# Performance work log

Measured on AMD Instinct MI355X. Metric: run time of the kernel, lower is better.

Reference implementation:

```python
import jax, jax.numpy as jnp
import numpy as np

N_HEADS = 16
HEAD_DIM = 128


def _rotate_half(x):
    x1, x2 = jnp.split(x, 2, axis=-1)
    return jnp.concatenate((-x2, x1), axis=-1)


def setup_inputs() -> dict:
    key = jax.random.key(0)
    ks = jax.random.split(key, 6)
    B, T, D = 2, 2048, 2048
    d = D // N_HEADS  # 128
    x = jax.random.normal(ks[0], (B, T, D), dtype=jnp.float32)
    # RoPE tables (shape [1,1,T,head_dim]) built as in standard implementations
    inv_freq = 1.0 / (10000.0 ** (jnp.arange(0, d, 2, dtype=jnp.float32) / d))
    ang = jnp.arange(T, dtype=jnp.float32)[:, None] * inv_freq[None, :]  # [T, d/2]
    emb = jnp.concatenate((ang, ang), axis=-1)  # [T, d]
    rope_cos = jnp.cos(emb)[None, None]
    rope_sin = jnp.sin(emb)[None, None]
    qkv_w = jax.random.normal(ks[1], (3 * D, D), dtype=jnp.float32) * (1.0 / np.sqrt(D))
    qkv_b = jnp.zeros((3 * D,), dtype=jnp.float32)
    out_w = jax.random.normal(ks[2], (D, D), dtype=jnp.float32) * (1.0 / np.sqrt(D))
    out_b = jnp.zeros((D,), dtype=jnp.float32)
    return {"x": x, "rope_cos": rope_cos, "rope_sin": rope_sin,
            "qkv_w": qkv_w, "qkv_b": qkv_b, "out_w": out_w, "out_b": out_b}


def reference(x, rope_cos, rope_sin, qkv_w, qkv_b, out_w, out_b):
    B, T, D = x.shape
    H, d = N_HEADS, D // N_HEADS
    # fused QKV projection: [B,T,3D] -> [3,B,H,T,d]
    qkv = (jnp.einsum('btd,ed->bte', x, qkv_w) + qkv_b)
    qkv = qkv.reshape(B, T, 3, H, d).transpose(2, 0, 3, 1, 4)
    q, k, v = qkv[0], qkv[1], qkv[2]
    cos = rope_cos[:, :, :T, :].astype(q.dtype)
    sin = rope_sin[:, :, :T, :].astype(q.dtype)
    q = q * cos + _rotate_half(q) * sin
    k = k * cos + _rotate_half(k) * sin
    # causal SDPA
    scale = 1.0 / jnp.sqrt(jnp.array(d, dtype=q.dtype))
    scores = jnp.einsum('bhqd,bhkd->bhqk', q, k) * scale  # [B,H,T,T]
    causal = jnp.tril(jnp.ones((T, T), dtype=bool))
    scores = jnp.where(causal, scores, jnp.finfo(scores.dtype).min)
    attn = jax.nn.softmax(scores, axis=-1)
    out = jnp.einsum('bhqk,bhkd->bhqd', attn, v)  # [B,H,T,d]
    out = out.transpose(0, 2, 1, 3).reshape(B, T, D)
    return jnp.einsum('btd,ed->bte', out, out_w) + out_b
```

## Files before the change

kernel.cpp:

```cpp
#include <hip/hip_runtime.h>
#include <cstdint>
#include <cstddef>

typedef unsigned short u16;
using bf16x8 = __attribute__((ext_vector_type(8))) short;
using f32x4  = __attribute__((ext_vector_type(4))) float;

#define MFMA16(a, b, c) __builtin_amdgcn_mfma_f32_16x16x32_bf16((a), (b), (c), 0, 0, 0)

__device__ __forceinline__ u16 f2bf(float f) {
  union { float f; unsigned u; } x; x.f = f;
  unsigned r = x.u + 0x7fffu + ((x.u >> 16) & 1u);
  return (u16)(r >> 16);
}
__device__ __forceinline__ float bf2f(u16 h) {
  union { unsigned u; float f; } x; x.u = ((unsigned)h) << 16;
  return x.f;
}
__device__ __forceinline__ void gll16(const void* g, void* l) {
  __builtin_amdgcn_global_load_lds((const __attribute__((address_space(1))) void*)g,
                                   (__attribute__((address_space(3))) void*)l, 16, 0, 0);
}

union U8 { bf16x8 v; u16 u[8]; };

__global__ __launch_bounds__(256) void cvt_kernel(const float* __restrict__ in,
                                                  u16* __restrict__ out, int n4) {
  int i = blockIdx.x * blockDim.x + threadIdx.x;
  if (i >= n4) return;
  float4 v = ((const float4*)in)[i];
  ushort4 o;
  o.x = f2bf(v.x); o.y = f2bf(v.y); o.z = f2bf(v.z); o.w = f2bf(v.w);
  ((ushort4*)out)[i] = o;
}

__global__ __launch_bounds__(256) void gemm_bt(const u16* __restrict__ A,
                                               const u16* __restrict__ Bw,
                                               const float* __restrict__ bias,
                                               void* __restrict__ Cout,
                                               int M, int N, int K, int out_bf16) {
  __shared__ u16 As[128 * 32];
  __shared__ u16 Bs[128 * 32];
  const int tid = threadIdx.x;
  const int lane = tid & 63, wave = tid >> 6;
  const int col = lane & 15, quad = lane >> 4;
  const int wr = wave >> 1, wc = wave & 1;
  const int bm = blockIdx.y, bn = blockIdx.x;
  const u16* Ag = A + (size_t)bm * 128 * K;
  const u16* Bg = Bw + (size_t)bn * 128 * K;
  f32x4 acc[4][4] = {};
  const int r0 = tid >> 2, kc = (tid & 3) * 8;
  for (int k0 = 0; k0 < K; k0 += 32) {
    __syncthreads();
    gll16(Ag + (size_t)r0 * K + k0 + kc,        (void*)(As + (size_t)tid * 8));
    gll16(Ag + (size_t)(r0 + 64) * K + k0 + kc, (void*)(As + (size_t)(256 + tid) * 8));
    gll16(Bg + (size_t)r0 * K + k0 + kc,        (void*)(Bs + (size_t)tid * 8));
    gll16(Bg + (size_t)(r0 + 64) * K + k0 + kc, (void*)(Bs + (size_t)(256 + tid) * 8));
    __syncthreads();
    bf16x8 af[4], bf[4];
#pragma unroll
    for (int i = 0; i < 4; i++) {
      af[i] = *(const bf16x8*)&As[(wr * 64 + i * 16 + col) * 32 + quad * 8];
      bf[i] = *(const bf16x8*)&Bs[(wc * 64 + i * 16 + col) * 32 + quad * 8];
    }
#pragma unroll
    for (int i = 0; i < 4; i++)
#pragma unroll
      for (int j = 0; j < 4; j++)
        acc[i][j] = MFMA16(af[i], bf[j], acc[i][j]);
  }
#pragma unroll
  for (int i = 0; i < 4; i++) {
    int row0 = bm * 128 + wr * 64 + i * 16 + quad * 4;
#pragma unroll
    for (int j = 0; j < 4; j++) {
      int cn = bn * 128 + wc * 64 + j * 16 + col;
      float bv = bias[cn];
#pragma unroll
      for (int r = 0; r < 4; r++) {
        float v = acc[i][j][r] + bv;
        size_t off = (size_t)(row0 + r) * N + cn;
        if (out_bf16) ((u16*)Cout)[off] = f2bf(v);
        else          ((float*)Cout)[off] = v;
      }
    }
  }
}

__global__ __launch_bounds__(256) void rope_kernel(const u16* __restrict__ qkv,
                                                   const float* __restrict__ cosT,
                                                   const float* __restrict__ sinT,
                                                   u16* __restrict__ qo,
                                                   u16* __restrict__ ko,
                                                   u16* __restrict__ vt) {
  __shared__ u16 vs[128 * 72];
  const int bh = blockIdx.x;
  const int b = bh >> 4, h = bh & 15;
  const int tb = blockIdx.y;
  const int tid = threadIdx.x;
  const int tl = tid >> 2;
  const int g = tid & 3;
  const int t = tb * 64 + tl;
  const size_t qrow = ((size_t)(b * 2048 + t)) * 6144 + h * 128;
  const size_t orow = ((size_t)bh * 2048 + t) * 128;
  const int tt = t * 128;
  const int dl = g * 16, dh = 64 + dl;
  const float scale = 0.08838834764831845f;
#pragma unroll
  for (int cch = 0; cch < 2; cch++) {
    const int o8 = cch * 8;
    U8 ql, qh, kl, kh, vl, vh;
    ql.v = *(const bf16x8*)&qkv[qrow + dl + o8];
    qh.v = *(const bf16x8*)&qkv[qrow + dh + o8];
    kl.v = *(const bf16x8*)&qkv[qrow + 2048 + dl + o8];
    kh.v = *(const bf16x8*)&qkv[qrow + 2048 + dh + o8];
    vl.v = *(const bf16x8*)&qkv[qrow + 4096 + dl + o8];
    vh.v = *(const bf16x8*)&qkv[qrow + 4096 + dh + o8];
    float cl[8], ch_[8], sl[8], sh_[8];
    *(float4*)&cl[0]  = *(const float4*)&cosT[tt + dl + o8];
    *(float4*)&cl[4]  = *(const float4*)&cosT[tt + dl + o8 + 4];
    *(float4*)&ch_[0] = *(const float4*)&cosT[tt + dh + o8];
    *(float4*)&ch_[4] = *(const float4*)&cosT[tt + dh + o8 + 4];
    *(float4*)&sl[0]  = *(const float4*)&sinT[tt + dl + o8];
    *(float4*)&sl[4]  = *(const float4*)&sinT[tt + dl + o8 + 4];
    *(float4*)&sh_[0] = *(const float4*)&sinT[tt + dh + o8];
    *(float4*)&sh_[4] = *(const float4*)&sinT[tt + dh + o8 + 4];
    U8 aq, bq, ak, bk;
#pragma unroll
    for (int i = 0; i < 8; i++) {
      float qlf = bf2f(ql.u[i]), qhf = bf2f(qh.u[i]);
      float klf = bf2f(kl.u[i]), khf = bf2f(kh.u[i]);
      aq.u[i] = f2bf((qlf * cl[i]  - qhf * sl[i])  * scale);
      bq.u[i] = f2bf((qhf * ch_[i] + qlf * sh_[i]) * scale);
      ak.u[i] = f2bf(klf * cl[i]  - khf * sl[i]);
      bk.u[i] = f2bf(khf * ch_[i] + klf * sh_[i]);
    }
    *(bf16x8*)&qo[orow + dl + o8] = aq.v;
    *(bf16x8*)&qo[orow + dh + o8] = bq.v;
    *(bf16x8*)&ko[orow + dl + o8] = ak.v;
    *(bf16x8*)&ko[orow + dh + o8] = bk.v;
#pragma unroll
    for (int i = 0; i < 8; i++) {
      vs[(dl + o8 + i) * 72 + tl] = vl.u[i];
      vs[(dh + o8 + i) * 72 + tl] = vh.u[i];
    }
  }
  __syncthreads();
#pragma unroll
  for (int c = 0; c < 4; c++) {
    int idx = c * 256 + tid;
    int dd = idx >> 3, chk = idx & 7;
    bf16x8 vv = *(const bf16x8*)&vs[dd * 72 + chk * 8];
    *(bf16x8*)&vt[((size_t)bh * 128 + dd) * 2048 + tb * 64 + chk * 8] = vv;
  }
}

__global__ __launch_bounds__(256) void attn_kernel(const u16* __restrict__ Q,
                                                   const u16* __restrict__ Kk,
                                                   const u16* __restrict__ Vt,
                                                   u16* __restrict__ O) {
  __shared__ u16 Ks[64 * 136];
  __shared__ u16 Vs[128 * 72];
  __shared__ u16 Ps[4][16 * 72];
  const int bh = blockIdx.y, b = bh >> 4, h = bh & 15;
  const int qtile = gridDim.x - 1 - blockIdx.x;
  const int qb = qtile * 128;
  const int tid = threadIdx.x, wave = tid >> 6, lane = tid & 63;
  const int col = lane & 15, quad = lane >> 4;
  const int qw0 = qb + wave * 32;
  const int qw1 = qw0 + 16;
  const u16* Qg = Q + (size_t)bh * 2048 * 128;
  const u16* Kg = Kk + (size_t)bh * 2048 * 128;
  const u16* Vg = Vt + (size_t)bh * 128 * 2048;
  bf16x8 qf0[4], qf1[4];
#pragma unroll
  for (int c = 0; c < 4; c++) {
    qf0[c] = *(const bf16x8*)&Qg[(size_t)(qw0 + col) * 128 + c * 32 + quad * 8];
    qf1[c] = *(const bf16x8*)&Qg[(size_t)(qw1 + col) * 128 + c * 32 + quad * 8];
  }
  f32x4 o0[8] = {}, o1[8] = {};
  float ls0[4] = {0.f, 0.f, 0.f, 0.f}, ls1[4] = {0.f, 0.f, 0.f, 0.f};
  const int ntiles = (qb + 128) >> 6;
  const int kr = tid >> 2, kc = (tid & 3) * 8;
  const int vr = tid >> 1, vc = (tid & 1) * 8;
  for (int it = 0; it < ntiles; ++it) {
    const int kt = it << 6;
    __syncthreads();
#pragma unroll
    for (int u = 0; u < 4; u++)
      *(bf16x8*)&Ks[kr * 136 + kc + u * 32] =
          *(const bf16x8*)&Kg[(size_t)(kt + kr) * 128 + kc + u * 32];
#pragma unroll
    for (int u = 0; u < 4; u++)
      *(bf16x8*)&Vs[vr * 72 + vc + u * 16] =
          *(const bf16x8*)&Vg[(size_t)vr * 2048 + kt + vc + u * 16];
    __syncthreads();
    if (kt > qw1 + 15) continue;
    const bool do0 = (kt <= qw0 + 15);
    f32x4 s0[4] = {}, s1[4] = {};
#pragma unroll
    for (int c = 0; c < 4; c++) {
#pragma unroll
      for (int kg = 0; kg < 4; kg++) {
        bf16x8 kf = *(const bf16x8*)&Ks[(kg * 16 + col) * 136 + c * 32 + quad * 8];
        s0[kg] = MFMA16(qf0[c], kf, s0[kg]);
        s1[kg] = MFMA16(qf1[c], kf, s1[kg]);
      }
    }
    u16* pw = Ps[wave];
    if (do0) {
#pragma unroll
      for (int kg = 0; kg < 4; kg++)
#pragma unroll
        for (int r = 0; r < 4; r++) {
          int key = kt + kg * 16 + col, qg = qw0 + quad * 4 + r;
          float p = (key <= qg) ? __expf(s0[kg][r]) : 0.f;
          ls0[r] += p;
          pw[(quad * 4 + r) * 72 + kg * 16 + col] = f2bf(p);
        }
#pragma unroll
      for (int ks = 0; ks < 64; ks += 32) {
        bf16x8 pf = *(const bf16x8*)&pw[col * 72 + ks + quad * 8];
#pragma unroll
        for (int dt = 0; dt < 8; dt++) {
          bf16x8 vf = *(const bf16x8*)&Vs[(dt * 16 + col) * 72 + ks + quad * 8];
          o0[dt] = MFMA16(pf, vf, o0[dt]);
        }
      }
    }
    {
#pragma unroll
      for (int kg = 0; kg < 4; kg++)
#pragma unroll
        for (int r = 0; r < 4; r++) {
          int key = kt + kg * 16 + col, qg = qw1 + quad * 4 + r;
          float p = (key <= qg) ? __expf(s1[kg][r]) : 0.f;
          ls1[r] += p;
          pw[(quad * 4 + r) * 72 + kg * 16 + col] = f2bf(p);
        }
#pragma unroll
      for (int ks = 0; ks < 64; ks += 32) {
        bf16x8 pf = *(const bf16x8*)&pw[col * 72 + ks + quad * 8];
#pragma unroll
        for (int dt = 0; dt < 8; dt++) {
          bf16x8 vf = *(const bf16x8*)&Vs[(dt * 16 + col) * 72 + ks + quad * 8];
          o1[dt] = MFMA16(pf, vf, o1[dt]);
        }
      }
    }
  }
#pragma unroll
  for (int st = 1; st < 16; st <<= 1)
#pragma unroll
    for (int r = 0; r < 4; r++) {
      ls0[r] += __shfl_xor(ls0[r], st);
      ls1[r] += __shfl_xor(ls1[r], st);
    }
#pragma unroll
  for (int r = 0; r < 4; r++) {
    float inv0 = 1.0f / ls0[r], inv1 = 1.0f / ls1[r];
    size_t row0 = ((size_t)(b * 2048 + qw0 + quad * 4 + r)) * 2048 + h * 128;
    size_t row1 = ((size_t)(b * 2048 + qw1 + quad * 4 + r)) * 2048 + h * 128;
#pragma unroll
    for (int dt = 0; dt < 8; dt++) {
      O[row0 + dt * 16 + col] = f2bf(o0[dt][r] * inv0);
      O[row1 + dt * 16 + col] = f2bf(o1[dt][r] * inv1);
    }
  }
}

extern "C" void kernel_launch(void* const* d_in, const int* in_sizes, int n_in,
                              void* d_out, int out_size, void* d_ws, size_t ws_size,
                              hipStream_t stream) {
  const float* x        = (const float*)d_in[0];
  const float* rope_cos = (const float*)d_in[1];
  const float* rope_sin = (const float*)d_in[2];
  const float* qkv_w    = (const float*)d_in[3];
  const float* qkv_b    = (const float*)d_in[4];
  const float* out_w    = (const float*)d_in[5];
  const float* out_b    = (const float*)d_in[6];
  float* out = (float*)d_out;
  u16* ws = (u16*)d_ws;
  u16* xb    = ws;
  u16* wqkvb = xb + 8388608;
  u16* woutb = wqkvb + 12582912;
  u16* qkvb  = woutb + 4194304;
  u16* qb    = qkvb + 25165824;
  u16* kb    = qb + 8388608;
  u16* vtb   = kb + 8388608;
  u16* attnb = xb;

  cvt_kernel<<<8192, 256, 0, stream>>>(x, xb, 2097152);
  cvt_kernel<<<12288, 256, 0, stream>>>(qkv_w, wqkvb, 3145728);
  cvt_kernel<<<4096, 256, 0, stream>>>(out_w, woutb, 1048576);
  gemm_bt<<<dim3(48, 32), 256, 0, stream>>>(xb, wqkvb, qkv_b, qkvb, 4096, 6144, 2048, 1);
  rope_kernel<<<dim3(32, 32), 256, 0, stream>>>(qkvb, rope_cos, rope_sin, qb, kb, vtb);
  attn_kernel<<<dim3(16, 32), 256, 0, stream>>>(qb, kb, vtb, attnb);
  gemm_bt<<<dim3(16, 32), 256, 0, stream>>>(attnb, woutb, out_b, out, 4096, 2048, 2048, 0);
}
```

Measured before the change: 466.4 us.

## Fuse RoPE and V transpose into QKV GEMM epilogue, merge casts, interleave PV MFMAs

The separate rope kernel is removed. The QKV GEMM epilogue now stages each 128x128 tile in shared memory, applies RoPE and the softmax scale for Q and K, and writes V transposed directly. This avoids writing and re-reading the bf16 QKV intermediate. The three fp32-to-bf16 casts are merged into one launch. In attention, both P fragments are built first so each V fragment load feeds two MFMAs, which halves the V LDS reads. The cost is a heavier GEMM epilogue and higher register pressure in the attention loop.

```diff
diff --git a/kernel.cpp b/kernel.cpp
--- a/kernel.cpp
+++ b/kernel.cpp
@@ -24,21 +24,139 @@
 
 union U8 { bf16x8 v; u16 u[8]; };
 
-__global__ __launch_bounds__(256) void cvt_kernel(const float* __restrict__ in,
-                                                  u16* __restrict__ out, int n4) {
+__global__ __launch_bounds__(256) void cvt3_kernel(const float* __restrict__ a, u16* __restrict__ oa, int na4,
+                                                   const float* __restrict__ bsrc, u16* __restrict__ ob, int nb4,
+                                                   const float* __restrict__ c, u16* __restrict__ oc, int nc4) {
   int i = blockIdx.x * blockDim.x + threadIdx.x;
-  if (i >= n4) return;
-  float4 v = ((const float4*)in)[i];
+  const float4* in; ushort4* out;
+  if (i < na4) { in = (const float4*)a + i; out = (ushort4*)oa + i; }
+  else if (i < na4 + nb4) { int j = i - na4; in = (const float4*)bsrc + j; out = (ushort4*)ob + j; }
+  else if (i < na4 + nb4 + nc4) { int j = i - na4 - nb4; in = (const float4*)c + j; out = (ushort4*)oc + j; }
+  else return;
+  float4 v = *in;
   ushort4 o;
   o.x = f2bf(v.x); o.y = f2bf(v.y); o.z = f2bf(v.z); o.w = f2bf(v.w);
-  ((ushort4*)out)[i] = o;
+  *out = o;
+}
+
+__global__ __launch_bounds__(256) void gemm_qkv_rope(const u16* __restrict__ A,
+                                                     const u16* __restrict__ Bw,
+                                                     const float* __restrict__ bias,
+                                                     const float* __restrict__ cosT,
+                                                     const float* __restrict__ sinT,
+                                                     u16* __restrict__ qo,
+                                                     u16* __restrict__ ko,
+                                                     u16* __restrict__ vt) {
+  __shared__ u16 smem[128 * 136];
+  u16* As = smem;
+  u16* Bs = smem + 8192;
+  const int K = 2048;
+  const int tid = threadIdx.x;
+  const int lane = tid & 63, wave = tid >> 6;
+  const int col = lane & 15, quad = lane >> 4;
+  const int wr = wave >> 1, wc = wave & 1;
+  const int bm = blockIdx.y, bn = blockIdx.x;
+  const u16* Ag = A + (size_t)bm * 128 * K;
+  const u16* Bg = Bw + (size_t)bn * 128 * K;
+  f32x4 acc[4][4] = {};
+  const int r0 = tid >> 2, kc = (tid & 3) * 8;
+  for (int k0 = 0; k0 < K; k0 += 32) {
+    __syncthreads();
+    gll16(Ag + (size_t)r0 * K + k0 + kc,        (void*)(As + (size_t)tid * 8));
+    gll16(Ag + (size_t)(r0 + 64) * K + k0 + kc, (void*)(As + (size_t)(256 + tid) * 8));
+    gll16(Bg + (size_t)r0 * K + k0 + kc,        (void*)(Bs + (size_t)tid * 8));
+    gll16(Bg + (size_t)(r0 + 64) * K + k0 + kc, (void*)(Bs + (size_t)(256 + tid) * 8));
+    __syncthreads();
+    bf16x8 af[4], bf[4];
+#pragma unroll
+    for (int i = 0; i < 4; i++) {
+      af[i] = *(const bf16x8*)&As[(wr * 64 + i * 16 + col) * 32 + quad * 8];
+      bf[i] = *(const bf16x8*)&Bs[(wc * 64 + i * 16 + col) * 32 + quad * 8];
+    }
+#pragma unroll
+    for (int i = 0; i < 4; i++)
+#pragma unroll
+      for (int j = 0; j < 4; j++)
+        acc[i][j] = MFMA16(af[i], bf[j], acc[i][j]);
+  }
+  const int proj = bn >> 4, h = bn & 15;
+  const int bloc = bm >> 4;
+  const int tbase = (bm & 15) * 128;
+  const size_t bh = (size_t)(bloc * 16 + h);
+  __syncthreads();
+  if (proj < 2) {
+#pragma unroll
+    for (int i = 0; i < 4; i++) {
+      int tr = wr * 64 + i * 16 + quad * 4;
+#pragma unroll
+      for (int j = 0; j < 4; j++) {
+        int cf = wc * 64 + j * 16 + col;
+        float bv = bias[bn * 128 + cf];
+#pragma unroll
+        for (int r = 0; r < 4; r++)
+          smem[(tr + r) * 136 + cf] = f2bf(acc[i][j][r] + bv);
+      }
+    }
+    __syncthreads();
+    const int t_l = tid >> 1, hseg = (tid & 1) * 32;
+    const int t = tbase + t_l;
+    u16* dst = proj ? ko : qo;
+    const float scale = proj ? 1.0f : 0.08838834764831845f;
+    size_t orow = (bh * 2048 + t) * 128;
+#pragma unroll
+    for (int c4 = 0; c4 < 4; c4++) {
+      int d0 = hseg + c4 * 8;
+      U8 lo, hi, olo, ohi;
+      lo.v = *(const bf16x8*)&smem[t_l * 136 + d0];
+      hi.v = *(const bf16x8*)&smem[t_l * 136 + d0 + 64];
+      float cl[8], ch_[8], sl[8], sh_[8];
+      *(float4*)&cl[0]  = *(const float4*)&cosT[t * 128 + d0];
+      *(float4*)&cl[4]  = *(const float4*)&cosT[t * 128 + d0 + 4];
+      *(float4*)&ch_[0] = *(const float4*)&cosT[t * 128 + d0 + 64];
+      *(float4*)&ch_[4] = *(const float4*)&cosT[t * 128 + d0 + 68];
+      *(float4*)&sl[0]  = *(const float4*)&sinT[t * 128 + d0];
+      *(float4*)&sl[4]  = *(const float4*)&sinT[t * 128 + d0 + 4];
+      *(float4*)&sh_[0] = *(const float4*)&sinT[t * 128 + d0 + 64];
+      *(float4*)&sh_[4] = *(const float4*)&sinT[t * 128 + d0 + 68];
+#pragma unroll
+      for (int e = 0; e < 8; e++) {
+        float l = bf2f(lo.u[e]), hv = bf2f(hi.u[e]);
+        olo.u[e] = f2bf((l * cl[e] - hv * sl[e]) * scale);
+        ohi.u[e] = f2bf((hv * ch_[e] + l * sh_[e]) * scale);
+      }
+      *(bf16x8*)&dst[orow + d0] = olo.v;
+      *(bf16x8*)&dst[orow + d0 + 64] = ohi.v;
+    }
+  } else {
+#pragma unroll
+    for (int i = 0; i < 4; i++) {
+      int t0 = wr * 64 + i * 16 + quad * 4;
+#pragma unroll
+      for (int j = 0; j < 4; j++) {
+        int d = wc * 64 + j * 16 + col;
+        float bv = bias[bn * 128 + d];
+        ushort4 pk;
+        pk.x = f2bf(acc[i][j][0] + bv);
+        pk.y = f2bf(acc[i][j][1] + bv);
+        pk.z = f2bf(acc[i][j][2] + bv);
+        pk.w = f2bf(acc[i][j][3] + bv);
+        *(ushort4*)&smem[d * 136 + t0] = pk;
+      }
+    }
+    __syncthreads();
+    const int d_l = tid >> 1, tseg = (tid & 1) * 64;
+    size_t vrow = (bh * 128 + d_l) * 2048 + tbase + tseg;
+#pragma unroll
+    for (int c8 = 0; c8 < 8; c8++)
+      *(bf16x8*)&vt[vrow + c8 * 8] = *(const bf16x8*)&smem[d_l * 136 + tseg + c8 * 8];
+  }
 }
 
 __global__ __launch_bounds__(256) void gemm_bt(const u16* __restrict__ A,
                                                const u16* __restrict__ Bw,
                                                const float* __restrict__ bias,
-                                               void* __restrict__ Cout,
-                                               int M, int N, int K, int out_bf16) {
+                                               float* __restrict__ Cout,
+                                               int M, int N, int K) {
   __shared__ u16 As[128 * 32];
   __shared__ u16 Bs[128 * 32];
   const int tid = threadIdx.x;
@@ -77,81 +195,9 @@
       int cn = bn * 128 + wc * 64 + j * 16 + col;
       float bv = bias[cn];
 #pragma unroll
-      for (int r = 0; r < 4; r++) {
-        float v = acc[i][j][r] + bv;
-        size_t off = (size_t)(row0 + r) * N + cn;
-        if (out_bf16) ((u16*)Cout)[off] = f2bf(v);
-        else          ((float*)Cout)[off] = v;
-      }
-    }
-  }
-}
-
-__global__ __launch_bounds__(256) void rope_kernel(const u16* __restrict__ qkv,
-                                                   const float* __restrict__ cosT,
-                                                   const float* __restrict__ sinT,
-                                                   u16* __restrict__ qo,
-                                                   u16* __restrict__ ko,
-                                                   u16* __restrict__ vt) {
-  __shared__ u16 vs[128 * 72];
-  const int bh = blockIdx.x;
-  const int b = bh >> 4, h = bh & 15;
-  const int tb = blockIdx.y;
-  const int tid = threadIdx.x;
-  const int tl = tid >> 2;
-  const int g = tid & 3;
-  const int t = tb * 64 + tl;
-  const size_t qrow = ((size_t)(b * 2048 + t)) * 6144 + h * 128;
-  const size_t orow = ((size_t)bh * 2048 + t) * 128;
-  const int tt = t * 128;
-  const int dl = g * 16, dh = 64 + dl;
-  const float scale = 0.08838834764831845f;
-#pragma unroll
-  for (int cch = 0; cch < 2; cch++) {
-    const int o8 = cch * 8;
-    U8 ql, qh, kl, kh, vl, vh;
-    ql.v = *(const bf16x8*)&qkv[qrow + dl + o8];
-    qh.v = *(const bf16x8*)&qkv[qrow + dh + o8];
-    kl.v = *(const bf16x8*)&qkv[qrow + 2048 + dl + o8];
-    kh.v = *(const bf16x8*)&qkv[qrow + 2048 + dh + o8];
-    vl.v = *(const bf16x8*)&qkv[qrow + 4096 + dl + o8];
-    vh.v = *(const bf16x8*)&qkv[qrow + 4096 + dh + o8];
-    float cl[8], ch_[8], sl[8], sh_[8];
-    *(float4*)&cl[0]  = *(const float4*)&cosT[tt + dl + o8];
-    *(float4*)&cl[4]  = *(const float4*)&cosT[tt + dl + o8 + 4];
-    *(float4*)&ch_[0] = *(const float4*)&cosT[tt + dh + o8];
-    *(float4*)&ch_[4] = *(const float4*)&cosT[tt + dh + o8 + 4];
-    *(float4*)&sl[0]  = *(const float4*)&sinT[tt + dl + o8];
-    *(float4*)&sl[4]  = *(const float4*)&sinT[tt + dl + o8 + 4];
-    *(float4*)&sh_[0] = *(const float4*)&sinT[tt + dh + o8];
-    *(float4*)&sh_[4] = *(const float4*)&sinT[tt + dh + o8 + 4];
-    U8 aq, bq, ak, bk;
-#pragma unroll
-    for (int i = 0; i < 8; i++) {
-      float qlf = bf2f(ql.u[i]), qhf = bf2f(qh.u[i]);
-      float klf = bf2f(kl.u[i]), khf = bf2f(kh.u[i]);
-      aq.u[i] = f2bf((qlf * cl[i]  - qhf * sl[i])  * scale);
-      bq.u[i] = f2bf((qhf * ch_[i] + qlf * sh_[i]) * scale);
-      ak.u[i] = f2bf(klf * cl[i]  - khf * sl[i]);
-      bk.u[i] = f2bf(khf * ch_[i] + klf * sh_[i]);
-    }
-    *(bf16x8*)&qo[orow + dl + o8] = aq.v;
-    *(bf16x8*)&qo[orow + dh + o8] = bq.v;
-    *(bf16x8*)&ko[orow + dl + o8] = ak.v;
-    *(bf16x8*)&ko[orow + dh + o8] = bk.v;
-#pragma unroll
-    for (int i = 0; i < 8; i++) {
-      vs[(dl + o8 + i) * 72 + tl] = vl.u[i];
-      vs[(dh + o8 + i) * 72 + tl] = vh.u[i];
-    }
-  }
-  __syncthreads();
-#pragma unroll
-  for (int c = 0; c < 4; c++) {
-    int idx = c * 256 + tid;
-    int dd = idx >> 3, chk = idx & 7;
-    bf16x8 vv = *(const bf16x8*)&vs[dd * 72 + chk * 8];
-    *(bf16x8*)&vt[((size_t)bh * 128 + dd) * 2048 + tb * 64 + chk * 8] = vv;
+      for (int r = 0; r < 4; r++)
+        Cout[(size_t)(row0 + r) * N + cn] = acc[i][j][r] + bv;
+    }
   }
 }
 
@@ -208,6 +254,7 @@
       }
     }
     u16* pw = Ps[wave];
+    bf16x8 pf0[2], pf1[2];
     if (do0) {
 #pragma unroll
       for (int kg = 0; kg < 4; kg++)
@@ -218,35 +265,37 @@
           ls0[r] += p;
           pw[(quad * 4 + r) * 72 + kg * 16 + col] = f2bf(p);
         }
-#pragma unroll
-      for (int ks = 0; ks < 64; ks += 32) {
-        bf16x8 pf = *(const bf16x8*)&pw[col * 72 + ks + quad * 8];
+      pf0[0] = *(const bf16x8*)&pw[col * 72 + quad * 8];
+      pf0[1] = *(const bf16x8*)&pw[col * 72 + 32 + quad * 8];
+    }
+#pragma unroll
+    for (int kg = 0; kg < 4; kg++)
+#pragma unroll
+      for (int r = 0; r < 4; r++) {
+        int key = kt + kg * 16 + col, qg = qw1 + quad * 4 + r;
+        float p = (key <= qg) ? __expf(s1[kg][r]) : 0.f;
+        ls1[r] += p;
+        pw[(quad * 4 + r) * 72 + kg * 16 + col] = f2bf(p);
+      }
+    pf1[0] = *(const bf16x8*)&pw[col * 72 + quad * 8];
+    pf1[1] = *(const bf16x8*)&pw[col * 72 + 32 + quad * 8];
+    if (do0) {
+#pragma unroll
+      for (int ks = 0; ks < 2; ks++)
 #pragma unroll
         for (int dt = 0; dt < 8; dt++) {
-          bf16x8 vf = *(const bf16x8*)&Vs[(dt * 16 + col) * 72 + ks + quad * 8];
-          o0[dt] = MFMA16(pf, vf, o0[dt]);
+          bf16x8 vf = *(const bf16x8*)&Vs[(dt * 16 + col) * 72 + ks * 32 + quad * 8];
+          o0[dt] = MFMA16(pf0[ks], vf, o0[dt]);
+          o1[dt] = MFMA16(pf1[ks], vf, o1[dt]);
         }
-      }
-    }
-    {
-#pragma unroll
-      for (int kg = 0; kg < 4; kg++)
-#pragma unroll
-        for (int r = 0; r < 4; r++) {
-          int key = kt + kg * 16 + col, qg = qw1 + quad * 4 + r;
-          float p = (key <= qg) ? __expf(s1[kg][r]) : 0.f;
-          ls1[r] += p;
-          pw[(quad * 4 + r) * 72 + kg * 16 + col] = f2bf(p);
+    } else {
+#pragma unroll
+      for (int ks = 0; ks < 2; ks++)
+#pragma unroll
+        for (int dt = 0; dt < 8; dt++) {
+          bf16x8 vf = *(const bf16x8*)&Vs[(dt * 16 + col) * 72 + ks * 32 + quad * 8];
+          o1[dt] = MFMA16(pf1[ks], vf, o1[dt]);
         }
-#pragma unroll
-      for (int ks = 0; ks < 64; ks += 32) {
-        bf16x8 pf = *(const bf16x8*)&pw[col * 72 + ks + quad * 8];
-#pragma unroll
-        for (int dt = 0; dt < 8; dt++) {
-          bf16x8 vf = *(const bf16x8*)&Vs[(dt * 16 + col) * 72 + ks + quad * 8];
-          o1[dt] = MFMA16(pf, vf, o1[dt]);
-        }
-      }
     }
   }
 #pragma unroll
@@ -284,17 +333,16 @@
   u16* xb    = ws;
   u16* wqkvb = xb + 8388608;
   u16* woutb = wqkvb + 12582912;
-  u16* qkvb  = woutb + 4194304;
-  u16* qb    = qkvb + 25165824;
+  u16* qb    = woutb + 4194304;
   u16* kb    = qb + 8388608;
   u16* vtb   = kb + 8388608;
   u16* attnb = xb;
 
-  cvt_kernel<<<8192, 256, 0, stream>>>(x, xb, 2097152);
-  cvt_kernel<<<12288, 256, 0, stream>>>(qkv_w, wqkvb, 3145728);
-  cvt_kernel<<<4096, 256, 0, stream>>>(out_w, woutb, 1048576);
-  gemm_bt<<<dim3(48, 32), 256, 0, stream>>>(xb, wqkvb, qkv_b, qkvb, 4096, 6144, 2048, 1);
-  rope_kernel<<<dim3(32, 32), 256, 0, stream>>>(qkvb, rope_cos, rope_sin, qb, kb, vtb);
+  cvt3_kernel<<<24576, 256, 0, stream>>>(x, xb, 2097152,
+                                         qkv_w, wqkvb, 3145728,
+                                         out_w, woutb, 1048576);
+  gemm_qkv_rope<<<dim3(48, 32), 256, 0, stream>>>(xb, wqkvb, qkv_b,
+                                                  rope_cos, rope_sin, qb, kb, vtb);
   attn_kernel<<<dim3(16, 32), 256, 0, stream>>>(qb, kb, vtb, attnb);
-  gemm_bt<<<dim3(16, 32), 256, 0, stream>>>(attnb, woutb, out_b, out, 4096, 2048, 2048, 0);
-}
+  gemm_bt<<<dim3(16, 32), 256, 0, stream>>>(attnb, woutb, out_b, out, 4096, 2048, 2048);
+}
```

Result: slower. 509.2 us (+9.2%).
